# Performance work log

Measured on AMD Instinct MI355X. Metric: run time of the kernel, lower is better.

## Reference

```python
import jax, jax.numpy as jnp
import numpy as np

NUM_KEYS = 8192
NUM_BINS = 128
NUM_FREQS = 64
NUM_KERNELS = 3
HEAD_DIM = 2 * NUM_FREQS


def setup_inputs() -> dict:
    key = jax.random.key(0)
    k1, k2, k3, k4, k5 = jax.random.split(key, 5)
    fan_in = NUM_FREQS * NUM_KERNELS
    bound = np.sqrt(6.0 / fan_in)
    return {
        "K": jax.random.normal(k1, (NUM_KEYS, HEAD_DIM), dtype=jnp.float32),
        "reference_angles": jax.random.normal(k2, (NUM_FREQS,), dtype=jnp.float32),
        "mu": jax.random.uniform(k3, (NUM_BINS, NUM_FREQS, NUM_KERNELS), minval=-1.0, maxval=1.0, dtype=jnp.float32),
        "kappa": jax.random.uniform(k4, (NUM_BINS, NUM_FREQS, NUM_KERNELS), minval=0.0, maxval=1.0, dtype=jnp.float32),
        "weight": jax.random.uniform(k5, (NUM_BINS, NUM_FREQS, NUM_KERNELS), minval=-bound, maxval=bound, dtype=jnp.float32),
        "bias": jnp.zeros((NUM_BINS,), dtype=jnp.float32),
    }


def reference(K, reference_angles, mu, kappa, weight, bias):
    n = K.shape[0]
    num_bins, num_freqs, num_kernels = mu.shape
    # split head_dim into (freq, 2) complex pairs
    Kc = K.reshape(n, num_freqs, 2)                      # (n, f, 2)
    magnitude = jnp.sqrt(jnp.sum(Kc * Kc, axis=2))       # (n, f)
    angle = jnp.arctan2(Kc[..., 1], Kc[..., 0])          # (n, f)
    # shift kernel centers by per-round reference angles
    mu_eff = mu + reference_angles[None, :, None]        # (b, f, k)
    # von Mises kernel: exp(kappa * (cos(angle - mu) - 1))
    # broadcast to (n, b, f, k) -- this is the fat intermediate
    delta = angle[:, None, :, None] - mu_eff[None]       # (n, b, f, k)
    kernel = jnp.exp(kappa[None] * (jnp.cos(delta) - 1.0))
    # sum over kernels with weights, then over freqs with magnitude
    wk = jnp.einsum('nbfk,bfk->nbf', kernel, weight)     # (n, b, f)
    logits = jnp.einsum('nbf,nf->nb', wk, magnitude)     # (n, b)
    return logits + bias[None, :]
```

## Files before the change

kernel.cpp:

```cpp
#include <hip/hip_runtime.h>
#include <math.h>

#define NKEYS 8192
#define NBINS 128
#define NFREQ 64
#define NKER  3
#define HEADD 128

#define MHARM 4
#define NCH   9
#define KDIM  (NCH * NFREQ)
#define KSTEPS (KDIM / 32)


#define BM 64
#define GT 256

typedef _Float16 f16x8 __attribute__((ext_vector_type(8)));
typedef float    f32x4 __attribute__((ext_vector_type(4)));

__global__ __launch_bounds__(GT, 2) void fused_all(
    const float* __restrict__ K,
    const float* __restrict__ refang,
    const float* __restrict__ mu,
    const float* __restrict__ kappa,
    const float* __restrict__ weight,
    const float* __restrict__ bias,
    float* __restrict__ out)
{
    __shared__ __align__(16) _Float16 Afrag[4 * KSTEPS * 512];

    const int tid  = threadIdx.x;
    const int bid  = blockIdx.x;
    const int row0 = (bid >> 1) * BM;
    const int cblk = bid & 1;

    #pragma unroll
    for (int it = 0; it < 2; ++it) {
        const int o  = tid + it * GT;
        const int n  = o >> 3, oc = o & 7;
        const int f0 = oc * 8;
        const int qa = oc & 3, half = oc >> 2;
        const int chunk = n >> 4, lcn = n & 15;
        const float* kp = K + (size_t)(row0 + n) * HEADD + 2 * f0;
        const float4 p0 = ((const float4*)kp)[0];
        const float4 p1 = ((const float4*)kp)[1];
        const float4 p2 = ((const float4*)kp)[2];
        const float4 p3 = ((const float4*)kp)[3];
        float xs[8] = {p0.x, p0.z, p1.x, p1.z, p2.x, p2.z, p3.x, p3.z};
        float ys[8] = {p0.y, p0.w, p1.y, p1.w, p2.y, p2.w, p3.y, p3.w};
        float mag[8], c1[8], cc[8], sc[8], cp[8], sp[8];
        #pragma unroll
        for (int i = 0; i < 8; ++i) {
            float m2 = xs[i] * xs[i] + ys[i] * ys[i];
            float ri = (m2 > 0.f) ? rsqrtf(m2) : 0.f;
            mag[i] = m2 * ri;
            c1[i] = xs[i] * ri;
            float s1 = ys[i] * ri;
            cp[i] = 1.f; sp[i] = 0.f; cc[i] = c1[i]; sc[i] = s1;
        }
        _Float16* base = Afrag + chunk * (KSTEPS * 512) + half * 512
                               + (qa * 16 + lcn) * 8;
        f16x8 v;
        #pragma unroll
        for (int i = 0; i < 8; ++i) v[i] = (_Float16)mag[i];
        *(f16x8*)base = v;
        #pragma unroll
        for (int m = 1; m <= MHARM; ++m) {
            f16x8 vc, vs;
            #pragma unroll
            for (int i = 0; i < 8; ++i) {
                vc[i] = (_Float16)(mag[i] * cc[i]);
                vs[i] = (_Float16)(mag[i] * sc[i]);
            }
            *(f16x8*)(base + (2 * m - 1) * 1024) = vc;
            *(f16x8*)(base + (2 * m) * 1024)     = vs;
            #pragma unroll
            for (int i = 0; i < 8; ++i) {
                float cn = fmaf(2.f * c1[i], cc[i], -cp[i]);
                float sn = fmaf(2.f * c1[i], sc[i], -sp[i]);
                cp[i] = cc[i]; sp[i] = sc[i]; cc[i] = cn; sc[i] = sn;
            }
        }
    }

    const int lane = tid & 63, wave = tid >> 6;
    const int q = lane >> 4, lc = lane & 15;
    const int g = cblk * 4 + wave;
    const int bin = g * 16 + lc;

    f16x8 bfrag[KSTEPS];
    #pragma unroll
    for (int half = 0; half < 2; ++half) {
        const int fb = half * 32 + q * 8;
        #pragma unroll
        for (int jq = 0; jq < 2; ++jq) {
            const size_t off = ((size_t)bin * NFREQ + fb + jq * 4) * NKER;
            const float4* mup = (const float4*)(mu + off);
            const float4* kpp = (const float4*)(kappa + off);
            const float4* wpp = (const float4*)(weight + off);
            float4 m4[3], k4[3], w4[3];
            #pragma unroll
            for (int i = 0; i < 3; ++i) { m4[i] = mup[i]; k4[i] = kpp[i]; w4[i] = wpp[i]; }
            const float* mv = (const float*)m4;
            const float* kv = (const float*)k4;
            const float* wv = (const float*)w4;
            #pragma unroll
            for (int jj = 0; jj < 4; ++jj) {
                const int j = jq * 4 + jj;
                const float rf = refang[fb + j];
                float ach[NCH];
                #pragma unroll
                for (int c = 0; c < NCH; ++c) ach[c] = 0.f;
                #pragma unroll
                for (int k = 0; k < NKER; ++k) {
                    const float me  = mv[3 * jj + k] + rf;
                    const float kap = kv[3 * jj + k];
                    const float w   = wv[3 * jj + k];
                    const float wek = w * __expf(-kap);
                    float s1, c1;
                    __sincosf(me, &s1, &c1);
                    const float h = 0.5f * kap, h2 = h * h;
                    {
                        float t = h2, s = 1.f + t;
                        t *= h2 * 0.25f;              s += t;
                        t *= h2 * (1.f / 9.f);        s += t;
                        ach[0] = fmaf(wek, s, ach[0]);
                    }
                    float cc = c1, sc = s1, cp = 1.f, sp = 0.f;
                    float tm = h;
                    #pragma unroll
                    for (int m = 1; m <= MHARM; ++m) {
                        float t = tm, s = tm;
                        t *= h2 * (1.f / (float)(1 * (m + 1))); s += t;
                        t *= h2 * (1.f / (float)(2 * (m + 2))); s += t;
                        t *= h2 * (1.f / (float)(3 * (m + 3))); s += t;
                        const float gm = 2.f * wek * s;
                        ach[2 * m - 1] = fmaf(gm, cc, ach[2 * m - 1]);
                        ach[2 * m]     = fmaf(gm, sc, ach[2 * m]);
                        const float cn = fmaf(2.f * c1, cc, -cp);
                        const float sn = fmaf(2.f * c1, sc, -sp);
                        cp = cc; sp = sc; cc = cn; sc = sn;
                        tm *= h * (1.f / (float)(m + 1));
                    }
                }
                #pragma unroll
                for (int c = 0; c < NCH; ++c)
                    bfrag[c * 2 + half][j] = (_Float16)ach[c];
            }
        }
    }

    __syncthreads();

    f32x4 acc[4] = {};
    const f16x8* ap = (const f16x8*)Afrag + lane;
    #pragma unroll
    for (int kt = 0; kt < KSTEPS; ++kt) {
        #pragma unroll
        for (int c = 0; c < 4; ++c) {
            f16x8 a = ap[c * (KSTEPS * 64) + kt * 64];
            acc[c] = __builtin_amdgcn_mfma_f32_16x16x32_f16(a, bfrag[kt], acc[c], 0, 0, 0);
        }
    }

    const int col = g * 16 + lc;
    const float bb = bias[col];
    #pragma unroll
    for (int c = 0; c < 4; ++c) {
        #pragma unroll
        for (int jj = 0; jj < 4; ++jj)
            out[(size_t)(row0 + c * 16 + q * 4 + jj) * NBINS + col] = acc[c][jj] + bb;
    }
}

extern "C" void kernel_launch(void* const* d_in, const int* in_sizes, int n_in,
                              void* d_out, int out_size, void* d_ws, size_t ws_size,
                              hipStream_t stream) {
    const float* K      = (const float*)d_in[0];
    const float* refang = (const float*)d_in[1];
    const float* mu     = (const float*)d_in[2];
    const float* kappa  = (const float*)d_in[3];
    const float* weight = (const float*)d_in[4];
    const float* bias   = (const float*)d_in[5];
    float* out = (float*)d_out;

    (void)d_ws; (void)ws_size; (void)in_sizes; (void)n_in; (void)out_size;

    fused_all<<<(NKEYS / BM) * 2, GT, 0, stream>>>(
        K, refang, mu, kappa, weight, bias, out);
}
```

Baseline: 15.65 us.

## Truncate harmonic expansion to 3 terms and halve rows per block

Reduces the Fourier/Bessel harmonic expansion of the von Mises kernel from 4 to 3 harmonics, which shrinks the GEMM K dimension from 9 to 7 channels per frequency. Halves the block row tile from 64 to 32, doubling the grid to 512 blocks, and restructures the B-fragment build to load 8 frequencies at once and compute the Bessel series per harmonic. The fewer harmonics cut both the B-fragment setup math and the MFMA work, but they loosen the approximation and may raise numerical error. Smaller tiles mean the per-block B-fragment computation, which is the dominant setup cost, is repeated across twice as many blocks.

```diff
diff --git a/kernel.cpp b/kernel.cpp
--- a/kernel.cpp
+++ b/kernel.cpp
@@ -7,13 +7,13 @@
 #define NKER  3
 #define HEADD 128
 
-#define MHARM 4
-#define NCH   9
+#define MHARM 3
+#define NCH   7
 #define KDIM  (NCH * NFREQ)
 #define KSTEPS (KDIM / 32)
 
 
-#define BM 64
+#define BM 32
 #define GT 256
 
 typedef _Float16 f16x8 __attribute__((ext_vector_type(8)));
@@ -28,42 +28,38 @@
     const float* __restrict__ bias,
     float* __restrict__ out)
 {
-    __shared__ __align__(16) _Float16 Afrag[4 * KSTEPS * 512];
+    __shared__ __align__(16) _Float16 Afrag[2 * KSTEPS * 512];
 
     const int tid  = threadIdx.x;
     const int bid  = blockIdx.x;
     const int row0 = (bid >> 1) * BM;
     const int cblk = bid & 1;
 
-    #pragma unroll
-    for (int it = 0; it < 2; ++it) {
-        const int o  = tid + it * GT;
-        const int n  = o >> 3, oc = o & 7;
-        const int f0 = oc * 8;
+    {
+        const int n  = tid >> 3;
+        const int oc = tid & 7;
         const int qa = oc & 3, half = oc >> 2;
         const int chunk = n >> 4, lcn = n & 15;
-        const float* kp = K + (size_t)(row0 + n) * HEADD + 2 * f0;
-        const float4 p0 = ((const float4*)kp)[0];
-        const float4 p1 = ((const float4*)kp)[1];
-        const float4 p2 = ((const float4*)kp)[2];
-        const float4 p3 = ((const float4*)kp)[3];
-        float xs[8] = {p0.x, p0.z, p1.x, p1.z, p2.x, p2.z, p3.x, p3.z};
-        float ys[8] = {p0.y, p0.w, p1.y, p1.w, p2.y, p2.w, p3.y, p3.w};
+
+        const float4* ldp = (const float4*)(K + (size_t)(row0 + n) * HEADD + oc * 16);
+        const float4 p0 = ldp[0], p1 = ldp[1], p2 = ldp[2], p3 = ldp[3];
+        const float xs[8] = {p0.x, p0.z, p1.x, p1.z, p2.x, p2.z, p3.x, p3.z};
+        const float ys[8] = {p0.y, p0.w, p1.y, p1.w, p2.y, p2.w, p3.y, p3.w};
+
         float mag[8], c1[8], cc[8], sc[8], cp[8], sp[8];
+        f16x8 v;
         #pragma unroll
         for (int i = 0; i < 8; ++i) {
-            float m2 = xs[i] * xs[i] + ys[i] * ys[i];
-            float ri = (m2 > 0.f) ? rsqrtf(m2) : 0.f;
+            const float m2 = xs[i] * xs[i] + ys[i] * ys[i];
+            const float ri = (m2 > 0.f) ? rsqrtf(m2) : 0.f;
             mag[i] = m2 * ri;
             c1[i] = xs[i] * ri;
-            float s1 = ys[i] * ri;
+            const float s1 = ys[i] * ri;
             cp[i] = 1.f; sp[i] = 0.f; cc[i] = c1[i]; sc[i] = s1;
+            v[i] = (_Float16)mag[i];
         }
         _Float16* base = Afrag + chunk * (KSTEPS * 512) + half * 512
                                + (qa * 16 + lcn) * 8;
-        f16x8 v;
-        #pragma unroll
-        for (int i = 0; i < 8; ++i) v[i] = (_Float16)mag[i];
         *(f16x8*)base = v;
         #pragma unroll
         for (int m = 1; m <= MHARM; ++m) {
@@ -72,15 +68,12 @@
             for (int i = 0; i < 8; ++i) {
                 vc[i] = (_Float16)(mag[i] * cc[i]);
                 vs[i] = (_Float16)(mag[i] * sc[i]);
+                const float cn = fmaf(2.f * c1[i], cc[i], -cp[i]);
+                const float sn = fmaf(2.f * c1[i], sc[i], -sp[i]);
+                cp[i] = cc[i]; sp[i] = sc[i]; cc[i] = cn; sc[i] = sn;
             }
             *(f16x8*)(base + (2 * m - 1) * 1024) = vc;
             *(f16x8*)(base + (2 * m) * 1024)     = vs;
-            #pragma unroll
-            for (int i = 0; i < 8; ++i) {
-                float cn = fmaf(2.f * c1[i], cc[i], -cp[i]);
-                float sn = fmaf(2.f * c1[i], sc[i], -sp[i]);
-                cp[i] = cc[i]; sp[i] = sc[i]; cc[i] = cn; sc[i] = sn;
-            }
         }
     }
 
@@ -93,84 +86,81 @@
     #pragma unroll
     for (int half = 0; half < 2; ++half) {
         const int fb = half * 32 + q * 8;
+        const size_t off = ((size_t)bin * NFREQ + fb) * NKER;
+        float4 m4[6], k4[6], w4[6];
         #pragma unroll
-        for (int jq = 0; jq < 2; ++jq) {
-            const size_t off = ((size_t)bin * NFREQ + fb + jq * 4) * NKER;
-            const float4* mup = (const float4*)(mu + off);
-            const float4* kpp = (const float4*)(kappa + off);
-            const float4* wpp = (const float4*)(weight + off);
-            float4 m4[3], k4[3], w4[3];
+        for (int i = 0; i < 6; ++i) {
+            m4[i] = ((const float4*)(mu + off))[i];
+            k4[i] = ((const float4*)(kappa + off))[i];
+            w4[i] = ((const float4*)(weight + off))[i];
+        }
+        const float* mv = (const float*)m4;
+        const float* kv = (const float*)k4;
+        const float* wv = (const float*)w4;
+        #pragma unroll
+        for (int j = 0; j < 8; ++j) {
+            const float rf = refang[fb + j];
+            float ach[NCH];
             #pragma unroll
-            for (int i = 0; i < 3; ++i) { m4[i] = mup[i]; k4[i] = kpp[i]; w4[i] = wpp[i]; }
-            const float* mv = (const float*)m4;
-            const float* kv = (const float*)k4;
-            const float* wv = (const float*)w4;
+            for (int c = 0; c < NCH; ++c) ach[c] = 0.f;
             #pragma unroll
-            for (int jj = 0; jj < 4; ++jj) {
-                const int j = jq * 4 + jj;
-                const float rf = refang[fb + j];
-                float ach[NCH];
+            for (int k = 0; k < NKER; ++k) {
+                const float me  = mv[3 * j + k] + rf;
+                const float kap = kv[3 * j + k];
+                const float w   = wv[3 * j + k];
+                const float wek = w * __expf(-kap);
+                float s1, c1;
+                __sincosf(me, &s1, &c1);
+                const float h = 0.5f * kap, h2 = h * h;
+
+                float Im[MHARM + 1];
+                float tm = 1.f;
                 #pragma unroll
-                for (int c = 0; c < NCH; ++c) ach[c] = 0.f;
+                for (int m = 0; m <= MHARM; ++m) {
+                    float t = tm, s = tm;
+                    #pragma unroll
+                    for (int jj = 1; jj <= 4; ++jj) { t *= h2 / (float)(jj * (m + jj)); s += t; }
+                    Im[m] = s;
+                    tm *= h / (float)(m + 1);
+                }
+
+                ach[0] = fmaf(wek, Im[0], ach[0]);
+                float cp = 1.f, sp = 0.f, cc = c1, sc = s1;
                 #pragma unroll
-                for (int k = 0; k < NKER; ++k) {
-                    const float me  = mv[3 * jj + k] + rf;
-                    const float kap = kv[3 * jj + k];
-                    const float w   = wv[3 * jj + k];
-                    const float wek = w * __expf(-kap);
-                    float s1, c1;
-                    __sincosf(me, &s1, &c1);
-                    const float h = 0.5f * kap, h2 = h * h;
-                    {
-                        float t = h2, s = 1.f + t;
-                        t *= h2 * 0.25f;              s += t;
-                        t *= h2 * (1.f / 9.f);        s += t;
-                        ach[0] = fmaf(wek, s, ach[0]);
-                    }
-                    float cc = c1, sc = s1, cp = 1.f, sp = 0.f;
-                    float tm = h;
-                    #pragma unroll
-                    for (int m = 1; m <= MHARM; ++m) {
-                        float t = tm, s = tm;
-                        t *= h2 * (1.f / (float)(1 * (m + 1))); s += t;
-                        t *= h2 * (1.f / (float)(2 * (m + 2))); s += t;
-                        t *= h2 * (1.f / (float)(3 * (m + 3))); s += t;
-                        const float gm = 2.f * wek * s;
-                        ach[2 * m - 1] = fmaf(gm, cc, ach[2 * m - 1]);
-                        ach[2 * m]     = fmaf(gm, sc, ach[2 * m]);
-                        const float cn = fmaf(2.f * c1, cc, -cp);
-                        const float sn = fmaf(2.f * c1, sc, -sp);
-                        cp = cc; sp = sc; cc = cn; sc = sn;
-                        tm *= h * (1.f / (float)(m + 1));
-                    }
+                for (int m = 1; m <= MHARM; ++m) {
+                    const float gm = 2.f * wek * Im[m];
+                    ach[2 * m - 1] = fmaf(gm, cc, ach[2 * m - 1]);
+                    ach[2 * m]     = fmaf(gm, sc, ach[2 * m]);
+                    const float cn = fmaf(2.f * c1, cc, -cp);
+                    const float sn = fmaf(2.f * c1, sc, -sp);
+                    cp = cc; sp = sc; cc = cn; sc = sn;
                 }
-                #pragma unroll
-                for (int c = 0; c < NCH; ++c)
-                    bfrag[c * 2 + half][j] = (_Float16)ach[c];
             }
+            #pragma unroll
+            for (int c = 0; c < NCH; ++c)
+                bfrag[c * 2 + half][j] = (_Float16)ach[c];
         }
     }
 
     __syncthreads();
 
-    f32x4 acc[4] = {};
+    f32x4 acc0 = {0.f, 0.f, 0.f, 0.f};
+    f32x4 acc1 = {0.f, 0.f, 0.f, 0.f};
     const f16x8* ap = (const f16x8*)Afrag + lane;
     #pragma unroll
     for (int kt = 0; kt < KSTEPS; ++kt) {
-        #pragma unroll
-        for (int c = 0; c < 4; ++c) {
-            f16x8 a = ap[c * (KSTEPS * 64) + kt * 64];
-            acc[c] = __builtin_amdgcn_mfma_f32_16x16x32_f16(a, bfrag[kt], acc[c], 0, 0, 0);
-        }
+        const f16x8 a0 = ap[kt * 64];
+        const f16x8 a1 = ap[KSTEPS * 64 + kt * 64];
+        acc0 = __builtin_amdgcn_mfma_f32_16x16x32_f16(a0, bfrag[kt], acc0, 0, 0, 0);
+        acc1 = __builtin_amdgcn_mfma_f32_16x16x32_f16(a1, bfrag[kt], acc1, 0, 0, 0);
     }
 
     const int col = g * 16 + lc;
     const float bb = bias[col];
     #pragma unroll
-    for (int c = 0; c < 4; ++c) {
-        #pragma unroll
-        for (int jj = 0; jj < 4; ++jj)
-            out[(size_t)(row0 + c * 16 + q * 4 + jj) * NBINS + col] = acc[c][jj] + bb;
+    for (int jj = 0; jj < 4; ++jj) {
+        out[(size_t)(row0 + q * 4 + jj) * NBINS + col]      = acc0[jj] + bb;
+        out[(size_t)(row0 + 16 + q * 4 + jj) * NBINS + col] = acc1[jj] + bb;
     }
 }
 
```

Result: slower. 38.09 us (+143.4%).
